# Performance work log

Measured on AMD Instinct MI355X. Metric: run time of the kernel, lower is better.

Reference implementation:

```python
import jax, jax.numpy as jnp
import numpy as np

DIM = 512
N = 1024          # num_patches == seq len
HEADS = 8
DIM_HEAD = 64
INNER = HEADS * DIM_HEAD
BATCH = 8


def setup_inputs() -> dict:
    key = jax.random.key(0)
    k1, k2, k3, k4, k5 = jax.random.split(key, 5)
    x = jax.random.normal(k1, (BATCH, N, DIM), dtype=jnp.float32)
    # nn.Linear(dim, inner*3, bias=False): store as [dim, 3*inner] for x @ W
    w_qkv = jax.random.normal(k2, (DIM, 3 * INNER), dtype=jnp.float32) * (DIM ** -0.5)
    # relative_bias_table: Parameter init'd to zeros in torch; use small randn so it matters
    bias_table = jax.random.normal(k3, (2 * N - 1, HEADS), dtype=jnp.float32) * 0.02
    w_out = jax.random.normal(k4, (INNER, DIM), dtype=jnp.float32) * (INNER ** -0.5)
    b_out = jax.random.normal(k5, (DIM,), dtype=jnp.float32) * 0.02
    return {"x": x, "w_qkv": w_qkv, "bias_table": bias_table, "w_out": w_out, "b_out": b_out}


def reference(x, w_qkv, bias_table, w_out, b_out):
    B, n, _ = x.shape
    scale = DIM_HEAD ** -0.5
    qkv = x @ w_qkv                                   # [B, n, 3*INNER]
    q, k, v = jnp.split(qkv, 3, axis=-1)
    def split_heads(t):
        return t.reshape(B, n, HEADS, DIM_HEAD).transpose(0, 2, 1, 3)  # [B, H, n, d]
    q, k, v = split_heads(q), split_heads(k), split_heads(v)
    dots = jnp.einsum('bhnd,bhmd->bhnm', q, k) * scale  # [B, H, n, n]
    # relative index: i - j + (n - 1)
    idx = jnp.arange(n)[:, None] - jnp.arange(n)[None, :] + (n - 1)  # [n, n]
    rel_bias = bias_table[idx]                        # [n, n, H]
    rel_bias = rel_bias.transpose(2, 0, 1)[None]      # [1, H, n, n]
    attn = jax.nn.softmax(dots + rel_bias, axis=-1)
    out = jnp.einsum('bhnm,bhmd->bhnd', attn, v)      # [B, H, n, d]
    out = out.transpose(0, 2, 1, 3).reshape(B, n, INNER)
    return out @ w_out + b_out
```

## Files before the change

### kernel.cpp

```cpp
#include <hip/hip_runtime.h>
#include <hip/hip_bf16.h>

typedef short bf16x8 __attribute__((ext_vector_type(8)));
typedef float floatx4 __attribute__((ext_vector_type(4)));
typedef float floatx16 __attribute__((ext_vector_type(16)));
typedef unsigned uintx4 __attribute__((ext_vector_type(4)));

typedef const __attribute__((address_space(1))) void gvoid_t;
typedef __attribute__((address_space(3))) void lvoid_t;

__device__ __forceinline__ void gload_lds16(const void* g, void* l) {
  __builtin_amdgcn_global_load_lds((gvoid_t*)g, (lvoid_t*)l, 16, 0, 0);
}

__device__ __forceinline__ unsigned short f2bf(float f) {
  union { float f; unsigned u; } c; c.f = f;
  unsigned u = c.u + 0x7FFFu + ((c.u >> 16) & 1u);
  return (unsigned short)(u >> 16);
}

#define LOG2E 1.44269504f
#define EXP2(x) __builtin_amdgcn_exp2f(x)

__device__ __forceinline__ float xmax32(float x) {
  float a = x, b;
  asm("v_mov_b32 %0, %1" : "=v"(b) : "v"(x));
  asm("v_permlane32_swap_b32 %0, %1" : "+v"(a), "+v"(b));
  return fmaxf(a, b);
}
__device__ __forceinline__ float xadd32(float x) {
  float a = x, b;
  asm("v_mov_b32 %0, %1" : "=v"(b) : "v"(x));
  asm("v_permlane32_swap_b32 %0, %1" : "+v"(a), "+v"(b));
  return a + b;
}

__global__ __launch_bounds__(256) void prep_kernel(
    const float* __restrict__ x,      unsigned short* __restrict__ xb,
    const float* __restrict__ w_qkv,  unsigned short* __restrict__ wqkvT,
    const float* __restrict__ w_out,  unsigned short* __restrict__ woutT,
    const float* __restrict__ btab,   float* __restrict__ btT) {
  const int bid = blockIdx.x;
  if (bid < 4096) {
    int i = bid * 256 + threadIdx.x;
    float4 v = ((const float4*)x)[i];
    ushort4 o;
    o.x = f2bf(v.x); o.y = f2bf(v.y); o.z = f2bf(v.z); o.w = f2bf(v.w);
    ((ushort4*)xb)[i] = o;
  } else if (bid < 7168) {
    int idx = (bid - 4096) * 256 + threadIdx.x;
    int k = idx / 1536, n = idx - k * 1536;
    wqkvT[n * 512 + k] = f2bf(w_qkv[idx]);
  } else if (bid < 8192) {
    int idx = (bid - 7168) * 256 + threadIdx.x;
    int k = idx >> 9, n = idx & 511;
    woutT[n * 512 + k] = f2bf(w_out[idx]);
  } else {
    int i = (bid - 8192) * 256 + threadIdx.x;
    if (i < 2047 * 8) {
      int idx = i >> 3, hh = i & 7;
      btT[hh * 2047 + idx] = btab[i] * LOG2E;
    }
  }
}

template <int EPI>
__global__ __launch_bounds__(256, 2) void gemm_bf16(
    const unsigned short* __restrict__ A,
    const unsigned short* __restrict__ Bt,
    int M, int N, int K,
    unsigned short* __restrict__ qo, unsigned short* __restrict__ ko,
    unsigned short* __restrict__ vo,
    float* __restrict__ out, const float* __restrict__ bias) {
  __shared__ alignas(16) unsigned short lA[128 * 64];
  __shared__ alignas(16) unsigned short lB[128 * 64];
  const int tid = threadIdx.x;
  const int wave = tid >> 6, lane = tid & 63;
  const int wr = wave >> 1, wc = wave & 1;
  const int lrow = lane & 15, lk = lane >> 4;
  const int m0 = blockIdx.x * 128, n0 = blockIdx.y * 128;

  floatx4 acc[4][4] = {};

  for (int k0 = 0; k0 < K; k0 += 64) {
    __syncthreads();
#pragma unroll
    for (int i = 0; i < 4; ++i) {
      int c = i * 256 + tid;
      int row = c >> 3, kc = c & 7;
      int ksw = (kc ^ (row & 7)) << 3;
      gload_lds16(A + (size_t)(m0 + row) * K + k0 + ksw,
                  &lA[(i * 256 + wave * 64) * 8]);
      gload_lds16(Bt + (size_t)(n0 + row) * K + k0 + ksw,
                  &lB[(i * 256 + wave * 64) * 8]);
    }
    __syncthreads();
#pragma unroll
    for (int f = 0; f < 2; ++f) {
      bf16x8 av[4], bv[4];
      int kc = lk + f * 4;
#pragma unroll
      for (int mt = 0; mt < 4; ++mt) {
        int r = wr * 64 + mt * 16 + lrow;
        av[mt] = *(const bf16x8*)&lA[r * 64 + ((kc ^ (r & 7)) << 3)];
      }
#pragma unroll
      for (int nt = 0; nt < 4; ++nt) {
        int r = wc * 64 + nt * 16 + lrow;
        bv[nt] = *(const bf16x8*)&lB[r * 64 + ((kc ^ (r & 7)) << 3)];
      }
#pragma unroll
      for (int mt = 0; mt < 4; ++mt)
#pragma unroll
        for (int nt = 0; nt < 4; ++nt)
          acc[mt][nt] = __builtin_amdgcn_mfma_f32_16x16x32_bf16(av[mt], bv[nt], acc[mt][nt], 0, 0, 0);
    }
  }

#pragma unroll
  for (int mt = 0; mt < 4; ++mt)
#pragma unroll
    for (int nt = 0; nt < 4; ++nt)
#pragma unroll
      for (int rg = 0; rg < 4; ++rg) {
        int m = m0 + wr * 64 + mt * 16 + lk * 4 + rg;
        int n = n0 + wc * 64 + nt * 16 + lrow;
        float v = acc[mt][nt][rg];
        if constexpr (EPI == 0) {
          int b = m >> 10, ii = m & 1023;
          int sect = n >> 9, r = n & 511;
          int h = r >> 6, d = r & 63;
          size_t bh = (size_t)((b << 3) + h);
          if (sect == 0)      qo[bh * 65536 + (size_t)ii * 64 + d] = f2bf(v * (0.125f * LOG2E));
          else if (sect == 1) ko[bh * 65536 + (size_t)ii * 64 + d] = f2bf(v);
          else                vo[bh * 65536 + (size_t)d * 1024 + ii] = f2bf(v);
        } else {
          out[(size_t)m * N + n] = v + bias[n];
        }
      }
}

__global__ __launch_bounds__(256, 3) void attn_kernel(
    const unsigned short* __restrict__ q,
    const unsigned short* __restrict__ kbuf,
    const unsigned short* __restrict__ vT,
    const float* __restrict__ btT,
    unsigned short* __restrict__ ao)
{
  __shared__ alignas(16) unsigned short lK[2][2][64 * 64];
  __shared__ float lbias[1088];
  const int tid = threadIdx.x, wave = tid >> 6, lane = tid & 63;
  const int il = lane & 31, hi = lane >> 5;
  const int pr = wave >> 1;
  const int wq = wave & 1;
  const int lid = ((blockIdx.x & 7) << 7) | (blockIdx.x >> 3);
  const int bh = lid >> 4, qt = lid & 15;
  const int h = bh & 7, b = bh >> 3;
  const int qB = qt * 64;
  const int i_ = qB + wq * 32 + il;
  const size_t base = (size_t)bh * 65536;
  const unsigned short* vrow = vT + base;

  for (int t = tid; t < 1087; t += 256)
    lbias[t] = btT[h * 2047 + qB + t];

  bf16x8 qf[4];
#pragma unroll
  for (int kd = 0; kd < 4; ++kd)
    qf[kd] = *(const bf16x8*)(q + base + (size_t)i_ * 64 + kd * 16 + hi * 8);

#define STAGE_K(dst, jbase)                                                     \
  {                                                                             \
    _Pragma("unroll") for (int i = 0; i < 4; ++i) {                             \
      int c = i * 128 + wq * 64 + lane;                                         \
      int row = c >> 3, kc = c & 7;                                             \
      gload_lds16(kbuf + base + (size_t)((jbase) + row) * 64 + ((kc ^ (row & 7)) << 3), \
                  &(dst)[(i * 128 + wq * 64) * 8]);                             \
    }                                                                           \
  }

  STAGE_K(lK[pr][0], pr * 512);
  __syncthreads();

  floatx16 accA = {}, accB = {};
  float m_ = -1e30f, s_ = 0.f;
  const int bias_off = (i_ - qB) + 1023 - 4 * hi;
  int buf = 0;

  for (int t = 0; t < 8; ++t) {
    const int j0 = pr * 512 + t * 64;
    if (t < 7) STAGE_K(lK[pr][buf ^ 1], j0 + 64);

    bf16x8 vf0[4], vf1[4];
#pragma unroll
    for (int ks = 0; ks < 4; ++ks) {
      vf0[ks] = *(const bf16x8*)(vrow + (size_t)il * 1024 + j0 + ks * 16 + hi * 8);
      vf1[ks] = *(const bf16x8*)(vrow + (size_t)(32 + il) * 1024 + j0 + ks * 16 + hi * 8);
    }

    floatx16 st0 = {}, st1 = {};
#pragma unroll
    for (int kd = 0; kd < 4; ++kd) {
      const int kc = ((kd * 2 + hi) ^ (il & 7)) << 3;
      bf16x8 kf0 = *(const bf16x8*)&lK[pr][buf][il * 64 + kc];
      bf16x8 kf1 = *(const bf16x8*)&lK[pr][buf][(32 + il) * 64 + kc];
      st0 = __builtin_amdgcn_mfma_f32_32x32x16_bf16(kf0, qf[kd], st0, 0, 0, 0);
      st1 = __builtin_amdgcn_mfma_f32_32x32x16_bf16(kf1, qf[kd], st1, 0, 0, 0);
    }

    const int bb = bias_off - j0;
    float pmp[4] = { -1e30f, -1e30f, -1e30f, -1e30f };
#pragma unroll
    for (int r = 0; r < 16; ++r) {
      const int jl = (r & 3) + 8 * (r >> 2);
      st0[r] += lbias[bb - jl];
      st1[r] += lbias[bb - 32 - jl];
      pmp[r & 3] = fmaxf(pmp[r & 3], fmaxf(st0[r], st1[r]));
    }
    float pm = fmaxf(fmaxf(pmp[0], pmp[1]), fmaxf(pmp[2], pmp[3]));
    pm = xmax32(pm);
    if (!__all(pm - m_ <= 8.f)) {
      const float nm = fmaxf(m_, pm);
      const float fs = EXP2(m_ - nm);
      s_ *= fs; accA *= fs; accB *= fs;
      m_ = nm;
    }
    float rsp[4] = { 0.f, 0.f, 0.f, 0.f };
#pragma unroll
    for (int r = 0; r < 16; ++r) {
      float e0 = EXP2(st0[r] - m_);
      float e1 = EXP2(st1[r] - m_);
      st0[r] = e0; st1[r] = e1;
      rsp[r & 3] += e0 + e1;
    }
    float rs = (rsp[0] + rsp[1]) + (rsp[2] + rsp[3]);
    s_ += xadd32(rs);

    unsigned pk[2][4][2];
#pragma unroll
    for (int g = 0; g < 4; ++g)
#pragma unroll
      for (int e2 = 0; e2 < 2; ++e2) {
        asm("v_cvt_pk_bf16_f32 %0, %1, %2"
            : "=v"(pk[0][g][e2]) : "v"(st0[4 * g + 2 * e2]), "v"(st0[4 * g + 2 * e2 + 1]));
        asm("v_cvt_pk_bf16_f32 %0, %1, %2"
            : "=v"(pk[1][g][e2]) : "v"(st1[4 * g + 2 * e2]), "v"(st1[4 * g + 2 * e2 + 1]));
      }
    bf16x8 pf[4];
#pragma unroll
    for (int ks = 0; ks < 4; ++ks) {
      const int jb = ks >> 1, gb = (ks & 1) * 2;
      uintx4 w;
#pragma unroll
      for (int e2 = 0; e2 < 2; ++e2) {
        unsigned d0 = pk[jb][gb][e2], d1 = pk[jb][gb + 1][e2];
        asm("v_permlane32_swap_b32 %0, %1" : "+v"(d0), "+v"(d1));
        w[e2]     = d0;
        w[2 + e2] = d1;
      }
      pf[ks] = *(bf16x8*)&w;
    }

#pragma unroll
    for (int ks = 0; ks < 4; ++ks) {
      accA = __builtin_amdgcn_mfma_f32_32x32x16_bf16(vf0[ks], pf[ks], accA, 0, 0, 0);
      accB = __builtin_amdgcn_mfma_f32_32x32x16_bf16(vf1[ks], pf[ks], accB, 0, 0, 0);
    }

    __syncthreads();
    buf ^= 1;
  }

  float* lu = (float*)&lK[0][0][0];
  if (wave >= 2) {
    float* slot = lu + (size_t)(wave - 2) * 2304 + lane * 36;
#pragma unroll
    for (int c = 0; c < 4; ++c) {
      floatx4 t4a = { accA[4 * c], accA[4 * c + 1], accA[4 * c + 2], accA[4 * c + 3] };
      floatx4 t4b = { accB[4 * c], accB[4 * c + 1], accB[4 * c + 2], accB[4 * c + 3] };
      *(floatx4*)(slot + 4 * c) = t4a;
      *(floatx4*)(slot + 16 + 4 * c) = t4b;
    }
    slot[32] = m_;
    slot[33] = s_;
  }
  __syncthreads();
  if (wave < 2) {
    const float* slot = lu + (size_t)wave * 2304 + lane * 36;
    floatx4 u2[8];
#pragma unroll
    for (int c = 0; c < 8; ++c) u2[c] = *(const floatx4*)(slot + 4 * c);
    const float m2 = slot[32], s2 = slot[33];
    const float mm = fmaxf(m_, m2);
    const float a0 = EXP2(m_ - mm), a1 = EXP2(m2 - mm);
    const float invs = 1.0f / (s_ * a0 + s2 * a1);
    const float c0 = a0 * invs, c1 = a1 * invs;

    unsigned short* aor = ao + (size_t)(b * 1024 + i_) * 512 + h * 64 + 4 * hi;
#pragma unroll
    for (int rq = 0; rq < 4; ++rq) {
      float oa0 = accA[4 * rq] * c0 + u2[rq][0] * c1;
      float oa1 = accA[4 * rq + 1] * c0 + u2[rq][1] * c1;
      float oa2 = accA[4 * rq + 2] * c0 + u2[rq][2] * c1;
      float oa3 = accA[4 * rq + 3] * c0 + u2[rq][3] * c1;
      float ob0 = accB[4 * rq] * c0 + u2[4 + rq][0] * c1;
      float ob1 = accB[4 * rq + 1] * c0 + u2[4 + rq][1] * c1;
      float ob2 = accB[4 * rq + 2] * c0 + u2[4 + rq][2] * c1;
      float ob3 = accB[4 * rq + 3] * c0 + u2[4 + rq][3] * c1;
      uint2 u;
      asm("v_cvt_pk_bf16_f32 %0, %1, %2" : "=v"(u.x) : "v"(oa0), "v"(oa1));
      asm("v_cvt_pk_bf16_f32 %0, %1, %2" : "=v"(u.y) : "v"(oa2), "v"(oa3));
      *(uint2*)(aor + 8 * rq) = u;
      asm("v_cvt_pk_bf16_f32 %0, %1, %2" : "=v"(u.x) : "v"(ob0), "v"(ob1));
      asm("v_cvt_pk_bf16_f32 %0, %1, %2" : "=v"(u.y) : "v"(ob2), "v"(ob3));
      *(uint2*)(aor + 32 + 8 * rq) = u;
    }
  }
}

extern "C" void kernel_launch(void* const* d_in, const int* in_sizes, int n_in,
                              void* d_out, int out_size, void* d_ws, size_t ws_size,
                              hipStream_t stream) {
  (void)in_sizes; (void)n_in; (void)out_size; (void)ws_size;
  const float* x      = (const float*)d_in[0];
  const float* w_qkv  = (const float*)d_in[1];
  const float* btab   = (const float*)d_in[2];
  const float* w_out  = (const float*)d_in[3];
  const float* b_out  = (const float*)d_in[4];
  float* out = (float*)d_out;

  char* ws = (char*)d_ws;
  unsigned short* xb    = (unsigned short*)(ws);
  unsigned short* wqkvT = (unsigned short*)(ws + 8388608);
  unsigned short* woutT = (unsigned short*)(ws + 9961472);
  unsigned short* qb    = (unsigned short*)(ws + 10485760);
  unsigned short* kb    = (unsigned short*)(ws + 18874368);
  unsigned short* vT    = (unsigned short*)(ws + 27262976);
  unsigned short* ao    = (unsigned short*)(ws + 35651584);
  float*          btT   = (float*)(ws + 44040192);

  hipLaunchKernelGGL(prep_kernel, dim3(8256), dim3(256), 0, stream,
                     x, xb, w_qkv, wqkvT, w_out, woutT, btab, btT);

  hipLaunchKernelGGL((gemm_bf16<0>), dim3(64, 12), dim3(256), 0, stream,
                     xb, wqkvT, 8192, 1536, 512, qb, kb, vT, (float*)nullptr, (const float*)nullptr);

  hipLaunchKernelGGL(attn_kernel, dim3(1024), dim3(256), 0, stream, qb, kb, vT, btT, ao);

  hipLaunchKernelGGL((gemm_bf16<1>), dim3(64, 4), dim3(256), 0, stream,
                     ao, woutT, 8192, 512, 512,
                     (unsigned short*)nullptr, (unsigned short*)nullptr, (unsigned short*)nullptr,
                     out, b_out);
}
```

Baseline: 100.2 us.

## Split attention KV range across three wave pairs instead of two

```diff
diff --git a/kernel.cpp b/kernel.cpp
--- a/kernel.cpp
+++ b/kernel.cpp
@@ -140,19 +140,21 @@
       }
 }
 
-__global__ __launch_bounds__(256, 3) void attn_kernel(
+__global__ __launch_bounds__(384, 3) void attn_kernel(
     const unsigned short* __restrict__ q,
     const unsigned short* __restrict__ kbuf,
     const unsigned short* __restrict__ vT,
     const float* __restrict__ btT,
     unsigned short* __restrict__ ao)
 {
-  __shared__ alignas(16) unsigned short lK[2][2][64 * 64];
+  __shared__ alignas(16) unsigned short lK[3][2][64 * 64];
   __shared__ float lbias[1088];
   const int tid = threadIdx.x, wave = tid >> 6, lane = tid & 63;
   const int il = lane & 31, hi = lane >> 5;
   const int pr = wave >> 1;
   const int wq = wave & 1;
+  const int myTiles = (pr == 0) ? 6 : 5;
+  const int tbase = (pr == 0) ? 0 : 1 + 5 * pr;
   const int lid = ((blockIdx.x & 7) << 7) | (blockIdx.x >> 3);
   const int bh = lid >> 4, qt = lid & 15;
   const int h = bh & 7, b = bh >> 3;
@@ -161,7 +163,7 @@
   const size_t base = (size_t)bh * 65536;
   const unsigned short* vrow = vT + base;
 
-  for (int t = tid; t < 1087; t += 256)
+  for (int t = tid; t < 1087; t += 384)
     lbias[t] = btT[h * 2047 + qB + t];
 
   bf16x8 qf[4];
@@ -179,7 +181,7 @@
     }                                                                           \
   }
 
-  STAGE_K(lK[pr][0], pr * 512);
+  STAGE_K(lK[pr][0], tbase * 64);
   __syncthreads();
 
   floatx16 accA = {}, accB = {};
@@ -187,84 +189,86 @@
   const int bias_off = (i_ - qB) + 1023 - 4 * hi;
   int buf = 0;
 
-  for (int t = 0; t < 8; ++t) {
-    const int j0 = pr * 512 + t * 64;
-    if (t < 7) STAGE_K(lK[pr][buf ^ 1], j0 + 64);
-
-    bf16x8 vf0[4], vf1[4];
-#pragma unroll
-    for (int ks = 0; ks < 4; ++ks) {
-      vf0[ks] = *(const bf16x8*)(vrow + (size_t)il * 1024 + j0 + ks * 16 + hi * 8);
-      vf1[ks] = *(const bf16x8*)(vrow + (size_t)(32 + il) * 1024 + j0 + ks * 16 + hi * 8);
-    }
-
-    floatx16 st0 = {}, st1 = {};
-#pragma unroll
-    for (int kd = 0; kd < 4; ++kd) {
-      const int kc = ((kd * 2 + hi) ^ (il & 7)) << 3;
-      bf16x8 kf0 = *(const bf16x8*)&lK[pr][buf][il * 64 + kc];
-      bf16x8 kf1 = *(const bf16x8*)&lK[pr][buf][(32 + il) * 64 + kc];
-      st0 = __builtin_amdgcn_mfma_f32_32x32x16_bf16(kf0, qf[kd], st0, 0, 0, 0);
-      st1 = __builtin_amdgcn_mfma_f32_32x32x16_bf16(kf1, qf[kd], st1, 0, 0, 0);
-    }
-
-    const int bb = bias_off - j0;
-    float pmp[4] = { -1e30f, -1e30f, -1e30f, -1e30f };
-#pragma unroll
-    for (int r = 0; r < 16; ++r) {
-      const int jl = (r & 3) + 8 * (r >> 2);
-      st0[r] += lbias[bb - jl];
-      st1[r] += lbias[bb - 32 - jl];
-      pmp[r & 3] = fmaxf(pmp[r & 3], fmaxf(st0[r], st1[r]));
-    }
-    float pm = fmaxf(fmaxf(pmp[0], pmp[1]), fmaxf(pmp[2], pmp[3]));
-    pm = xmax32(pm);
-    if (!__all(pm - m_ <= 8.f)) {
-      const float nm = fmaxf(m_, pm);
-      const float fs = EXP2(m_ - nm);
-      s_ *= fs; accA *= fs; accB *= fs;
-      m_ = nm;
-    }
-    float rsp[4] = { 0.f, 0.f, 0.f, 0.f };
-#pragma unroll
-    for (int r = 0; r < 16; ++r) {
-      float e0 = EXP2(st0[r] - m_);
-      float e1 = EXP2(st1[r] - m_);
-      st0[r] = e0; st1[r] = e1;
-      rsp[r & 3] += e0 + e1;
-    }
-    float rs = (rsp[0] + rsp[1]) + (rsp[2] + rsp[3]);
-    s_ += xadd32(rs);
-
-    unsigned pk[2][4][2];
-#pragma unroll
-    for (int g = 0; g < 4; ++g)
-#pragma unroll
-      for (int e2 = 0; e2 < 2; ++e2) {
-        asm("v_cvt_pk_bf16_f32 %0, %1, %2"
-            : "=v"(pk[0][g][e2]) : "v"(st0[4 * g + 2 * e2]), "v"(st0[4 * g + 2 * e2 + 1]));
-        asm("v_cvt_pk_bf16_f32 %0, %1, %2"
-            : "=v"(pk[1][g][e2]) : "v"(st1[4 * g + 2 * e2]), "v"(st1[4 * g + 2 * e2 + 1]));
-      }
-    bf16x8 pf[4];
-#pragma unroll
-    for (int ks = 0; ks < 4; ++ks) {
-      const int jb = ks >> 1, gb = (ks & 1) * 2;
-      uintx4 w;
-#pragma unroll
-      for (int e2 = 0; e2 < 2; ++e2) {
-        unsigned d0 = pk[jb][gb][e2], d1 = pk[jb][gb + 1][e2];
-        asm("v_permlane32_swap_b32 %0, %1" : "+v"(d0), "+v"(d1));
-        w[e2]     = d0;
-        w[2 + e2] = d1;
-      }
-      pf[ks] = *(bf16x8*)&w;
-    }
-
-#pragma unroll
-    for (int ks = 0; ks < 4; ++ks) {
-      accA = __builtin_amdgcn_mfma_f32_32x32x16_bf16(vf0[ks], pf[ks], accA, 0, 0, 0);
-      accB = __builtin_amdgcn_mfma_f32_32x32x16_bf16(vf1[ks], pf[ks], accB, 0, 0, 0);
+  for (int t = 0; t < 6; ++t) {
+    if (t < myTiles) {
+      const int j0 = (tbase + t) * 64;
+      if (t + 1 < myTiles) STAGE_K(lK[pr][buf ^ 1], j0 + 64);
+
+      bf16x8 vf0[4], vf1[4];
+#pragma unroll
+      for (int ks = 0; ks < 4; ++ks) {
+        vf0[ks] = *(const bf16x8*)(vrow + (size_t)il * 1024 + j0 + ks * 16 + hi * 8);
+        vf1[ks] = *(const bf16x8*)(vrow + (size_t)(32 + il) * 1024 + j0 + ks * 16 + hi * 8);
+      }
+
+      floatx16 st0 = {}, st1 = {};
+#pragma unroll
+      for (int kd = 0; kd < 4; ++kd) {
+        const int kc = ((kd * 2 + hi) ^ (il & 7)) << 3;
+        bf16x8 kf0 = *(const bf16x8*)&lK[pr][buf][il * 64 + kc];
+        bf16x8 kf1 = *(const bf16x8*)&lK[pr][buf][(32 + il) * 64 + kc];
+        st0 = __builtin_amdgcn_mfma_f32_32x32x16_bf16(kf0, qf[kd], st0, 0, 0, 0);
+        st1 = __builtin_amdgcn_mfma_f32_32x32x16_bf16(kf1, qf[kd], st1, 0, 0, 0);
+      }
+
+      const int bb = bias_off - j0;
+      float pmp[4] = { -1e30f, -1e30f, -1e30f, -1e30f };
+#pragma unroll
+      for (int r = 0; r < 16; ++r) {
+        const int jl = (r & 3) + 8 * (r >> 2);
+        st0[r] += lbias[bb - jl];
+        st1[r] += lbias[bb - 32 - jl];
+        pmp[r & 3] = fmaxf(pmp[r & 3], fmaxf(st0[r], st1[r]));
+      }
+      float pm = fmaxf(fmaxf(pmp[0], pmp[1]), fmaxf(pmp[2], pmp[3]));
+      pm = xmax32(pm);
+      if (!__all(pm - m_ <= 8.f)) {
+        const float nm = fmaxf(m_, pm);
+        const float fs = EXP2(m_ - nm);
+        s_ *= fs; accA *= fs; accB *= fs;
+        m_ = nm;
+      }
+      float rsp[4] = { 0.f, 0.f, 0.f, 0.f };
+#pragma unroll
+      for (int r = 0; r < 16; ++r) {
+        float e0 = EXP2(st0[r] - m_);
+        float e1 = EXP2(st1[r] - m_);
+        st0[r] = e0; st1[r] = e1;
+        rsp[r & 3] += e0 + e1;
+      }
+      float rs = (rsp[0] + rsp[1]) + (rsp[2] + rsp[3]);
+      s_ += xadd32(rs);
+
+      unsigned pk[2][4][2];
+#pragma unroll
+      for (int g = 0; g < 4; ++g)
+#pragma unroll
+        for (int e2 = 0; e2 < 2; ++e2) {
+          asm("v_cvt_pk_bf16_f32 %0, %1, %2"
+              : "=v"(pk[0][g][e2]) : "v"(st0[4 * g + 2 * e2]), "v"(st0[4 * g + 2 * e2 + 1]));
+          asm("v_cvt_pk_bf16_f32 %0, %1, %2"
+              : "=v"(pk[1][g][e2]) : "v"(st1[4 * g + 2 * e2]), "v"(st1[4 * g + 2 * e2 + 1]));
+        }
+      bf16x8 pf[4];
+#pragma unroll
+      for (int ks = 0; ks < 4; ++ks) {
+        const int jb = ks >> 1, gb = (ks & 1) * 2;
+        uintx4 w;
+#pragma unroll
+        for (int e2 = 0; e2 < 2; ++e2) {
+          unsigned d0 = pk[jb][gb][e2], d1 = pk[jb][gb + 1][e2];
+          asm("v_permlane32_swap_b32 %0, %1" : "+v"(d0), "+v"(d1));
+          w[e2]     = d0;
+          w[2 + e2] = d1;
+        }
+        pf[ks] = *(bf16x8*)&w;
+      }
+
+#pragma unroll
+      for (int ks = 0; ks < 4; ++ks) {
+        accA = __builtin_amdgcn_mfma_f32_32x32x16_bf16(vf0[ks], pf[ks], accA, 0, 0, 0);
+        accB = __builtin_amdgcn_mfma_f32_32x32x16_bf16(vf1[ks], pf[ks], accB, 0, 0, 0);
+      }
     }
 
     __syncthreads();
@@ -273,7 +277,7 @@
 
   float* lu = (float*)&lK[0][0][0];
   if (wave >= 2) {
-    float* slot = lu + (size_t)(wave - 2) * 2304 + lane * 36;
+    float* slot = lu + ((size_t)(wave - 2) * 64 + lane) * 36;
 #pragma unroll
     for (int c = 0; c < 4; ++c) {
       floatx4 t4a = { accA[4 * c], accA[4 * c + 1], accA[4 * c + 2], accA[4 * c + 3] };
@@ -286,27 +290,29 @@
   }
   __syncthreads();
   if (wave < 2) {
-    const float* slot = lu + (size_t)wave * 2304 + lane * 36;
-    floatx4 u2[8];
-#pragma unroll
-    for (int c = 0; c < 8; ++c) u2[c] = *(const floatx4*)(slot + 4 * c);
-    const float m2 = slot[32], s2 = slot[33];
-    const float mm = fmaxf(m_, m2);
-    const float a0 = EXP2(m_ - mm), a1 = EXP2(m2 - mm);
-    const float invs = 1.0f / (s_ * a0 + s2 * a1);
-    const float c0 = a0 * invs, c1 = a1 * invs;
+    const float* s1 = lu + ((size_t)wave * 64 + lane) * 36;
+    const float* s2 = lu + ((size_t)(2 + wave) * 64 + lane) * 36;
+    floatx4 u1[8], u2[8];
+#pragma unroll
+    for (int c = 0; c < 8; ++c) { u1[c] = *(const floatx4*)(s1 + 4 * c); u2[c] = *(const floatx4*)(s2 + 4 * c); }
+    const float m1 = s1[32], ss1 = s1[33];
+    const float m2 = s2[32], ss2 = s2[33];
+    const float mm = fmaxf(m_, fmaxf(m1, m2));
+    const float c0 = EXP2(m_ - mm), c1 = EXP2(m1 - mm), c2 = EXP2(m2 - mm);
+    const float inv = 1.0f / (c0 * s_ + c1 * ss1 + c2 * ss2);
+    const float d0 = c0 * inv, d1 = c1 * inv, d2 = c2 * inv;
 
     unsigned short* aor = ao + (size_t)(b * 1024 + i_) * 512 + h * 64 + 4 * hi;
 #pragma unroll
     for (int rq = 0; rq < 4; ++rq) {
-      float oa0 = accA[4 * rq] * c0 + u2[rq][0] * c1;
-      float oa1 = accA[4 * rq + 1] * c0 + u2[rq][1] * c1;
-      float oa2 = accA[4 * rq + 2] * c0 + u2[rq][2] * c1;
-      float oa3 = accA[4 * rq + 3] * c0 + u2[rq][3] * c1;
-      float ob0 = accB[4 * rq] * c0 + u2[4 + rq][0] * c1;
-      float ob1 = accB[4 * rq + 1] * c0 + u2[4 + rq][1] * c1;
-      float ob2 = accB[4 * rq + 2] * c0 + u2[4 + rq][2] * c1;
-      float ob3 = accB[4 * rq + 3] * c0 + u2[4 + rq][3] * c1;
+      float oa0 = accA[4 * rq] * d0 + u1[rq][0] * d1 + u2[rq][0] * d2;
+      float oa1 = accA[4 * rq + 1] * d0 + u1[rq][1] * d1 + u2[rq][1] * d2;
+      float oa2 = accA[4 * rq + 2] * d0 + u1[rq][2] * d1 + u2[rq][2] * d2;
+      float oa3 = accA[4 * rq + 3] * d0 + u1[rq][3] * d1 + u2[rq][3] * d2;
+      float ob0 = accB[4 * rq] * d0 + u1[4 + rq][0] * d1 + u2[4 + rq][0] * d2;
+      float ob1 = accB[4 * rq + 1] * d0 + u1[4 + rq][1] * d1 + u2[4 + rq][1] * d2;
+      float ob2 = accB[4 * rq + 2] * d0 + u1[4 + rq][2] * d1 + u2[4 + rq][2] * d2;
+      float ob3 = accB[4 * rq + 3] * d0 + u1[4 + rq][3] * d1 + u2[4 + rq][3] * d2;
       uint2 u;
       asm("v_cvt_pk_bf16_f32 %0, %1, %2" : "=v"(u.x) : "v"(oa0), "v"(oa1));
       asm("v_cvt_pk_bf16_f32 %0, %1, %2" : "=v"(u.y) : "v"(oa2), "v"(oa3));
@@ -345,7 +351,7 @@
   hipLaunchKernelGGL((gemm_bf16<0>), dim3(64, 12), dim3(256), 0, stream,
                      xb, wqkvT, 8192, 1536, 512, qb, kb, vT, (float*)nullptr, (const float*)nullptr);
 
-  hipLaunchKernelGGL(attn_kernel, dim3(1024), dim3(256), 0, stream, qb, kb, vT, btT, ao);
+  hipLaunchKernelGGL(attn_kernel, dim3(1024), dim3(384), 0, stream, qb, kb, vT, btT, ao);
 
   hipLaunchKernelGGL((gemm_bf16<1>), dim3(64, 4), dim3(256), 0, stream,
                      ao, woutT, 8192, 512, 512,
```

New measurement: 111.1 us. 10.9% more time.

## Load K tiles directly into registers instead of staging through LDS

Applied to the files above, without the earlier changes.

```diff
diff --git a/kernel.cpp b/kernel.cpp
--- a/kernel.cpp
+++ b/kernel.cpp
@@ -147,7 +147,7 @@
     const float* __restrict__ btT,
     unsigned short* __restrict__ ao)
 {
-  __shared__ alignas(16) unsigned short lK[2][2][64 * 64];
+  __shared__ alignas(16) float lu[2 * 64 * 36];
   __shared__ float lbias[1088];
   const int tid = threadIdx.x, wave = tid >> 6, lane = tid & 63;
   const int il = lane & 31, hi = lane >> 5;
@@ -160,6 +160,7 @@
   const int i_ = qB + wq * 32 + il;
   const size_t base = (size_t)bh * 65536;
   const unsigned short* vrow = vT + base;
+  const unsigned short* krow = kbuf + base;
 
   for (int t = tid; t < 1087; t += 256)
     lbias[t] = btT[h * 2047 + qB + t];
@@ -169,27 +170,25 @@
   for (int kd = 0; kd < 4; ++kd)
     qf[kd] = *(const bf16x8*)(q + base + (size_t)i_ * 64 + kd * 16 + hi * 8);
 
-#define STAGE_K(dst, jbase)                                                     \
-  {                                                                             \
-    _Pragma("unroll") for (int i = 0; i < 4; ++i) {                             \
-      int c = i * 128 + wq * 64 + lane;                                         \
-      int row = c >> 3, kc = c & 7;                                             \
-      gload_lds16(kbuf + base + (size_t)((jbase) + row) * 64 + ((kc ^ (row & 7)) << 3), \
-                  &(dst)[(i * 128 + wq * 64) * 8]);                             \
-    }                                                                           \
-  }
-
-  STAGE_K(lK[pr][0], pr * 512);
   __syncthreads();
 
   floatx16 accA = {}, accB = {};
   float m_ = -1e30f, s_ = 0.f;
   const int bias_off = (i_ - qB) + 1023 - 4 * hi;
-  int buf = 0;
-
+
+  bf16x8 kc0[4], kc1[4];
+  {
+    const int j0 = pr * 512;
+#pragma unroll
+    for (int kd = 0; kd < 4; ++kd) {
+      kc0[kd] = *(const bf16x8*)(krow + (size_t)(j0 + il) * 64 + kd * 16 + hi * 8);
+      kc1[kd] = *(const bf16x8*)(krow + (size_t)(j0 + 32 + il) * 64 + kd * 16 + hi * 8);
+    }
+  }
+
+#pragma unroll
   for (int t = 0; t < 8; ++t) {
     const int j0 = pr * 512 + t * 64;
-    if (t < 7) STAGE_K(lK[pr][buf ^ 1], j0 + 64);
 
     bf16x8 vf0[4], vf1[4];
 #pragma unroll
@@ -197,15 +196,21 @@
       vf0[ks] = *(const bf16x8*)(vrow + (size_t)il * 1024 + j0 + ks * 16 + hi * 8);
       vf1[ks] = *(const bf16x8*)(vrow + (size_t)(32 + il) * 1024 + j0 + ks * 16 + hi * 8);
     }
+    bf16x8 kn0[4], kn1[4];
+    if (t < 7) {
+      const int jn = j0 + 64;
+#pragma unroll
+      for (int kd = 0; kd < 4; ++kd) {
+        kn0[kd] = *(const bf16x8*)(krow + (size_t)(jn + il) * 64 + kd * 16 + hi * 8);
+        kn1[kd] = *(const bf16x8*)(krow + (size_t)(jn + 32 + il) * 64 + kd * 16 + hi * 8);
+      }
+    }
 
     floatx16 st0 = {}, st1 = {};
 #pragma unroll
     for (int kd = 0; kd < 4; ++kd) {
-      const int kc = ((kd * 2 + hi) ^ (il & 7)) << 3;
-      bf16x8 kf0 = *(const bf16x8*)&lK[pr][buf][il * 64 + kc];
-      bf16x8 kf1 = *(const bf16x8*)&lK[pr][buf][(32 + il) * 64 + kc];
-      st0 = __builtin_amdgcn_mfma_f32_32x32x16_bf16(kf0, qf[kd], st0, 0, 0, 0);
-      st1 = __builtin_amdgcn_mfma_f32_32x32x16_bf16(kf1, qf[kd], st1, 0, 0, 0);
+      st0 = __builtin_amdgcn_mfma_f32_32x32x16_bf16(kc0[kd], qf[kd], st0, 0, 0, 0);
+      st1 = __builtin_amdgcn_mfma_f32_32x32x16_bf16(kc1[kd], qf[kd], st1, 0, 0, 0);
     }
 
     const int bb = bias_off - j0;
@@ -267,11 +272,12 @@
       accB = __builtin_amdgcn_mfma_f32_32x32x16_bf16(vf1[ks], pf[ks], accB, 0, 0, 0);
     }
 
-    __syncthreads();
-    buf ^= 1;
-  }
-
-  float* lu = (float*)&lK[0][0][0];
+    if (t < 7) {
+#pragma unroll
+      for (int kd = 0; kd < 4; ++kd) { kc0[kd] = kn0[kd]; kc1[kd] = kn1[kd]; }
+    }
+  }
+
   if (wave >= 2) {
     float* slot = lu + (size_t)(wave - 2) * 2304 + lane * 36;
 #pragma unroll
```

Result: slower. 131.3 us (+31.1%).
